# Performance work log

Hardware: AMD Instinct MI355X
Metric: run time of the kernel (lower is better)

## Reference

```python
import jax, jax.numpy as jnp
import numpy as np

B, N, M, C, H, D = 1, 4096, 4096, 768, 12, 64  # batch, tgt len, src len, in_dim, heads, head_dim
SCALE = D ** -0.5


def setup_inputs() -> dict:
    key = jax.random.key(0)
    ks = jax.random.split(key, 6)
    s = 0.02
    return {
        "x": jax.random.normal(ks[0], (B, N, C), jnp.float32),
        "src": jax.random.normal(ks[1], (B, M, C), jnp.float32),
        "W_qv": jax.random.normal(ks[2], (2 * H * D, C), jnp.float32) * s,
        "W_k": jax.random.normal(ks[3], (H * D, C), jnp.float32) * s,
        "W_proj": jax.random.normal(ks[4], (C, H * D), jnp.float32) * s,
        "b_proj": jnp.zeros((C,), jnp.float32),
    }


def reference(x, src, W_qv, W_k, W_proj, b_proj):
    Bb, Nn, _ = x.shape
    Mm = src.shape[1]
    # q, v come from src; k comes from x (info flows src -> target)
    qv = (src @ W_qv.T).reshape(Bb, Mm, 2, H, D)
    q = qv[:, :, 0].transpose(0, 2, 1, 3)  # (B, H, M, D)
    v = qv[:, :, 1].transpose(0, 2, 1, 3)  # (B, H, M, D)
    k = (x @ W_k.T).reshape(Bb, Nn, H, D) * SCALE  # (B, N, H, D), pre-scaled
    # attn[b,h,n,m] = q[b,h,m,:] . k[b,n,h,:]  (torch: (q @ k).transpose(-2,-1))
    attn = jnp.einsum('bhmd,bnhd->bhnm', q, k)
    attn = jax.nn.softmax(attn, axis=-1)  # softmax over src tokens m
    y = jnp.einsum('bhnm,bhmd->bnhd', attn, v).reshape(Bb, Nn, H * D)
    return y @ W_proj.T + b_proj
```

## Files before the change

### kernel.cpp

```cpp
#include <hip/hip_runtime.h>

using f32x4 = __attribute__((ext_vector_type(4))) float;
using f32x16 = __attribute__((ext_vector_type(16))) float;
using s16x8 = __attribute__((ext_vector_type(8))) short;
using u16x4 = __attribute__((ext_vector_type(4))) unsigned short;
using u32x4 = __attribute__((ext_vector_type(4))) unsigned int;

#define AS1 __attribute__((address_space(1)))
#define AS3 __attribute__((address_space(3)))

__device__ __forceinline__ void gload16(const void* g, void* l) {
  __builtin_amdgcn_global_load_lds((const AS1 unsigned int*)g,
                                   (AS3 unsigned int*)l, 16, 0, 0);
}

__device__ __forceinline__ unsigned short f2bf(float f) {
  unsigned int u = __builtin_bit_cast(unsigned int, f);
  u += 0x7fffu + ((u >> 16) & 1u);
  return (unsigned short)(u >> 16);
}

__device__ __forceinline__ float b2f(unsigned short u) {
  unsigned int x = ((unsigned int)u) << 16;
  return __builtin_bit_cast(float, x);
}

__device__ __forceinline__ unsigned int cvtpk(float lo, float hi) {
  unsigned int w;
  asm("v_cvt_pk_bf16_f32 %0, %1, %2" : "=v"(w) : "v"(lo), "v"(hi));
  return w;
}

__device__ __forceinline__ void plswap(unsigned int& a, unsigned int& b) {
  asm("v_permlane32_swap_b32 %0, %1" : "+v"(a), "+v"(b));
}

__global__ __launch_bounds__(256) void cvt_bf16_multi(
    const float* __restrict__ i0, const float* __restrict__ i1,
    const float* __restrict__ i2, const float* __restrict__ i3,
    const float* __restrict__ i4, unsigned short* __restrict__ o0,
    unsigned short* __restrict__ o1, unsigned short* __restrict__ o2,
    unsigned short* __restrict__ o3, unsigned short* __restrict__ o4) {
  int b = blockIdx.x;
  const float* in;
  unsigned short* out;
  int base, n4;
  if (b < 3072) { in = i0; out = o0; base = b; n4 = 786432; }
  else if (b < 6144) { in = i1; out = o1; base = b - 3072; n4 = 786432; }
  else if (b < 7296) { in = i2; out = o2; base = b - 6144; n4 = 294912; }
  else if (b < 7872) { in = i3; out = o3; base = b - 7296; n4 = 147456; }
  else { in = i4; out = o4; base = b - 7872; n4 = 147456; }
  int i = base * 256 + threadIdx.x;
  if (i >= n4) return;
  f32x4 v = ((const f32x4*)in)[i];
  u16x4 r;
#pragma unroll
  for (int j = 0; j < 4; ++j) r[j] = f2bf(v[j]);
  ((u16x4*)out)[i] = r;
}

__global__ __launch_bounds__(256) void gemm_proj(
    const unsigned short* __restrict__ srcb, const unsigned short* __restrict__ wqvb,
    const unsigned short* __restrict__ xb, const unsigned short* __restrict__ wkb,
    unsigned short* __restrict__ qbuf, unsigned short* __restrict__ vtbuf,
    unsigned short* __restrict__ kbuf) {
  __shared__ __align__(16) unsigned short As[128 * 64];
  __shared__ __align__(16) unsigned short Bs[128 * 64];
  const bool isqv = blockIdx.y < 12;
  const unsigned short* A = isqv ? srcb : xb;
  const unsigned short* B = isqv ? wqvb : wkb;
  const int n0 = (isqv ? blockIdx.y : (blockIdx.y - 12)) * 128;
  const int m0 = blockIdx.x * 128;
  const int t = threadIdx.x;
  const int lane = t & 63;
  const int wid = t >> 6;
  const int wr = wid >> 1, wc = wid & 1;
  const int fr = lane & 15, fq = lane >> 4;

  f32x4 acc[4][4];
#pragma unroll
  for (int i = 0; i < 4; ++i)
#pragma unroll
    for (int j = 0; j < 4; ++j) acc[i][j] = (f32x4){0.f, 0.f, 0.f, 0.f};

  const char* Ab = (const char*)A;
  const char* Bb = (const char*)B;

  for (int k0 = 0; k0 < 768; k0 += 64) {
#pragma unroll
    for (int p = 0; p < 4; ++p) {
      int idx = p * 256 + t;
      int row = idx >> 3;
      int scb = ((idx & 7) << 4) ^ ((row & 7) << 4);
      char* dstA = (char*)As + (p * 256 + (wid << 6)) * 16;
      char* dstB = (char*)Bs + (p * 256 + (wid << 6)) * 16;
      gload16(Ab + (size_t)(m0 + row) * 1536 + (size_t)k0 * 2 + scb, dstA);
      gload16(Bb + (size_t)(n0 + row) * 1536 + (size_t)k0 * 2 + scb, dstB);
    }
    __syncthreads();

    s16x8 af[4][2], bfr[4][2];
#pragma unroll
    for (int mi = 0; mi < 4; ++mi)
#pragma unroll
      for (int kk = 0; kk < 2; ++kk) {
        int row = wr * 64 + mi * 16 + fr;
        int cb = (kk * 64 + (fq << 4)) ^ ((row & 7) << 4);
        af[mi][kk] = *(const s16x8*)((const char*)As + row * 128 + cb);
      }
#pragma unroll
    for (int ni = 0; ni < 4; ++ni)
#pragma unroll
      for (int kk = 0; kk < 2; ++kk) {
        int row = wc * 64 + ni * 16 + fr;
        int cb = (kk * 64 + (fq << 4)) ^ ((row & 7) << 4);
        bfr[ni][kk] = *(const s16x8*)((const char*)Bs + row * 128 + cb);
      }
    __builtin_amdgcn_s_setprio(1);
#pragma unroll
    for (int kk = 0; kk < 2; ++kk)
#pragma unroll
      for (int mi = 0; mi < 4; ++mi)
#pragma unroll
        for (int ni = 0; ni < 4; ++ni)
          acc[mi][ni] = __builtin_amdgcn_mfma_f32_16x16x32_bf16(
              af[mi][kk], bfr[ni][kk], acc[mi][ni], 0, 0, 0);
    __builtin_amdgcn_s_setprio(0);
    __syncthreads();
  }

#pragma unroll
  for (int mi = 0; mi < 4; ++mi) {
#pragma unroll
    for (int ni = 0; ni < 4; ++ni) {
      int row0 = m0 + wr * 64 + mi * 16 + (fq << 2);
      int col = n0 + wc * 64 + ni * 16 + fr;
      if (isqv) {
        if (n0 < 768) {
#pragma unroll
          for (int j = 0; j < 4; ++j)
            qbuf[(size_t)(row0 + j) * 768 + col] = f2bf(acc[mi][ni][j]);
        } else {
          u16x4 pk;
#pragma unroll
          for (int j = 0; j < 4; ++j) pk[j] = f2bf(acc[mi][ni][j]);
          *(u16x4*)(vtbuf + (size_t)(col - 768) * 4096 + row0) = pk;
        }
      } else {
#pragma unroll
        for (int j = 0; j < 4; ++j)
          kbuf[(size_t)(row0 + j) * 768 + col] = f2bf(acc[mi][ni][j] * 0.18033688f);
      }
    }
  }
}

__global__ __launch_bounds__(256) void gemm_out(
    const unsigned short* __restrict__ A, const unsigned short* __restrict__ B,
    float* __restrict__ outp, const float* __restrict__ bias) {
  __shared__ __align__(16) unsigned short As[64 * 64];
  __shared__ __align__(16) unsigned short Bs[64 * 64];
  const int t = threadIdx.x;
  const int lane = t & 63;
  const int wid = t >> 6;
  const int wr = wid >> 1, wc = wid & 1;
  const int m0 = blockIdx.x * 64, n0 = blockIdx.y * 64;
  const int fr = lane & 15, fq = lane >> 4;

  f32x4 acc[2][2];
#pragma unroll
  for (int i = 0; i < 2; ++i)
#pragma unroll
    for (int j = 0; j < 2; ++j) acc[i][j] = (f32x4){0.f, 0.f, 0.f, 0.f};

  for (int k0 = 0; k0 < 768; k0 += 64) {
#pragma unroll
    for (int p = 0; p < 2; ++p) {
      int idx = p * 256 + t;
      int row = idx >> 3;
      int scb = ((idx & 7) << 4) ^ ((row & 7) << 4);
      char* dstA = (char*)As + (p * 256 + (wid << 6)) * 16;
      char* dstB = (char*)Bs + (p * 256 + (wid << 6)) * 16;
      gload16((const char*)A + (size_t)(m0 + row) * 1536 + (size_t)k0 * 2 + scb, dstA);
      gload16((const char*)B + (size_t)(n0 + row) * 1536 + (size_t)k0 * 2 + scb, dstB);
    }
    __syncthreads();

    s16x8 af[2][2], bfr[2][2];
#pragma unroll
    for (int mi = 0; mi < 2; ++mi)
#pragma unroll
      for (int kk = 0; kk < 2; ++kk) {
        int row = wr * 32 + mi * 16 + fr;
        int cb = (kk * 64 + (fq << 4)) ^ ((row & 7) << 4);
        af[mi][kk] = *(const s16x8*)((const char*)As + row * 128 + cb);
      }
#pragma unroll
    for (int ni = 0; ni < 2; ++ni)
#pragma unroll
      for (int kk = 0; kk < 2; ++kk) {
        int row = wc * 32 + ni * 16 + fr;
        int cb = (kk * 64 + (fq << 4)) ^ ((row & 7) << 4);
        bfr[ni][kk] = *(const s16x8*)((const char*)Bs + row * 128 + cb);
      }
    __builtin_amdgcn_s_setprio(1);
#pragma unroll
    for (int kk = 0; kk < 2; ++kk)
#pragma unroll
      for (int mi = 0; mi < 2; ++mi)
#pragma unroll
        for (int ni = 0; ni < 2; ++ni)
          acc[mi][ni] = __builtin_amdgcn_mfma_f32_16x16x32_bf16(
              af[mi][kk], bfr[ni][kk], acc[mi][ni], 0, 0, 0);
    __builtin_amdgcn_s_setprio(0);
    __syncthreads();
  }

#pragma unroll
  for (int mi = 0; mi < 2; ++mi) {
#pragma unroll
    for (int ni = 0; ni < 2; ++ni) {
      int row0 = m0 + wr * 32 + mi * 16 + (fq << 2);
      int col = n0 + wc * 32 + ni * 16 + fr;
      float bv = bias[col];
#pragma unroll
      for (int j = 0; j < 4; ++j)
        outp[(size_t)(row0 + j) * 768 + col] = acc[mi][ni][j] + bv;
    }
  }
}

__global__ __launch_bounds__(256, 3) void attn_kernel(
    const unsigned short* __restrict__ Qk, const unsigned short* __restrict__ Kq,
    const unsigned short* __restrict__ Vt, unsigned short* __restrict__ Po0,
    unsigned short* __restrict__ PoR, float* __restrict__ Pl) {
  __shared__ __align__(16) unsigned short Ks[3][64 * 64];
  __shared__ __align__(16) unsigned short Vs[3][64 * 64];
  const int t = threadIdx.x, lane = t & 63, wid = t >> 6;
  const int half = lane >> 5, l31 = lane & 31;

  int bid = blockIdx.x;
  int f = (bid & 7) * 192 + (bid >> 3);
  const int h = f >> 7;
  const int rem = f & 127;
  const int n0 = (rem >> 2) * 128;
  const int sp = rem & 3;
  const int mbase = sp * 1024;

  s16x8 qf[4];
  {
    const size_t qrow = n0 + wid * 32 + l31;
#pragma unroll
    for (int kc = 0; kc < 4; ++kc)
      qf[kc] = *(const s16x8*)(Qk + qrow * 768 + h * 64 + kc * 16 + half * 8);
  }

  f32x16 o[2];
#pragma unroll
  for (int dt = 0; dt < 2; ++dt)
#pragma unroll
    for (int r = 0; r < 16; ++r) o[dt][r] = 0.f;
  f32x16 lacc;
#pragma unroll
  for (int r = 0; r < 16; ++r) lacc[r] = 0.f;
  f32x16 z16;
#pragma unroll
  for (int r = 0; r < 16; ++r) z16[r] = 0.f;
  s16x8 ones;
#pragma unroll
  for (int i = 0; i < 8; ++i) ones[i] = (short)0x3F80;

  const int rswz = (l31 & 7) << 4;
  const int rbase = l31 * 128;
  int coff[4];
#pragma unroll
  for (int kc = 0; kc < 4; ++kc)
    coff[kc] = (kc * 32 + half * 16) ^ rswz;

  const int srow = t >> 3;
  const int sscb = ((t & 7) << 4) ^ ((srow & 7) << 4);
  const char* kp0 = (const char*)Kq + (size_t)(mbase + srow) * 1536 + h * 128 + sscb;
  const char* kp1 = kp0 + 49152;
  const char* vp0 = (const char*)Vt + (size_t)(h * 64 + srow) * 8192 +
                    (size_t)mbase * 2 + sscb;
  const char* vp1 = vp0 + 262144;
  const int ldst = wid << 10;

#pragma unroll
  for (int pb = 0; pb < 2; ++pb) {
    char* kd = (char*)Ks + pb * 8192 + ldst;
    char* vd = (char*)Vs + pb * 8192 + ldst;
    gload16(kp0, kd);
    gload16(kp1, kd + 4096);
    gload16(vp0, vd);
    gload16(vp1, vd + 4096);
    kp0 += 98304; kp1 += 98304; vp0 += 128; vp1 += 128;
  }

  int cur = 0;
  for (int it = 0; it < 16; ++it) {
    if (it < 15) {
      asm volatile("s_waitcnt vmcnt(4)" ::: "memory");
    } else {
      asm volatile("s_waitcnt vmcnt(0)" ::: "memory");
    }
    __builtin_amdgcn_s_barrier();
    __builtin_amdgcn_sched_barrier(0);

    if (it < 14) {
      int stg = cur + 2;
      if (stg >= 3) stg -= 3;
      char* kd = (char*)Ks + stg * 8192 + ldst;
      char* vd = (char*)Vs + stg * 8192 + ldst;
      gload16(kp0, kd);
      gload16(kp1, kd + 4096);
      gload16(vp0, vd);
      gload16(vp1, vd + 4096);
      kp0 += 98304; kp1 += 98304; vp0 += 128; vp1 += 128;
    }

    const char* Ksb = (const char*)Ks + cur * 8192;
    const char* Vsb = (const char*)Vs + cur * 8192;

    s16x8 pfrag[4];
#pragma unroll
    for (int mt = 0; mt < 2; ++mt) {
      f32x16 s;
      __builtin_amdgcn_s_setprio(1);
      {
        s16x8 kf = *(const s16x8*)(Ksb + mt * 4096 + rbase + coff[0]);
        s = __builtin_amdgcn_mfma_f32_32x32x16_bf16(kf, qf[0], z16, 0, 0, 0);
      }
#pragma unroll
      for (int kc = 1; kc < 4; ++kc) {
        s16x8 kf = *(const s16x8*)(Ksb + mt * 4096 + rbase + coff[kc]);
        s = __builtin_amdgcn_mfma_f32_32x32x16_bf16(kf, qf[kc], s, 0, 0, 0);
      }
      __builtin_amdgcn_s_setprio(0);

#pragma unroll
      for (int r = 0; r < 16; ++r) s[r] = __builtin_exp2f(s[r]);

      unsigned int w[8];
#pragma unroll
      for (int i = 0; i < 8; ++i) w[i] = cvtpk(s[2 * i], s[2 * i + 1]);
      plswap(w[0], w[2]);
      plswap(w[1], w[3]);
      plswap(w[4], w[6]);
      plswap(w[5], w[7]);
      u32x4 f0, f1;
      f0[0] = w[0]; f0[1] = w[1]; f0[2] = w[2]; f0[3] = w[3];
      f1[0] = w[4]; f1[1] = w[5]; f1[2] = w[6]; f1[3] = w[7];
      pfrag[2 * mt] = __builtin_bit_cast(s16x8, f0);
      pfrag[2 * mt + 1] = __builtin_bit_cast(s16x8, f1);

      __builtin_amdgcn_s_setprio(1);
      lacc = __builtin_amdgcn_mfma_f32_32x32x16_bf16(ones, pfrag[2 * mt], lacc, 0, 0, 0);
      lacc = __builtin_amdgcn_mfma_f32_32x32x16_bf16(ones, pfrag[2 * mt + 1], lacc, 0, 0, 0);
      __builtin_amdgcn_s_setprio(0);
    }

    __builtin_amdgcn_s_setprio(1);
#pragma unroll
    for (int dt = 0; dt < 2; ++dt)
#pragma unroll
      for (int kc = 0; kc < 4; ++kc) {
        s16x8 vf = *(const s16x8*)(Vsb + dt * 4096 + rbase + coff[kc]);
        o[dt] = __builtin_amdgcn_mfma_f32_32x32x16_bf16(vf, pfrag[kc], o[dt], 0, 0, 0);
      }
    __builtin_amdgcn_s_setprio(0);

    cur = (cur == 2) ? 0 : cur + 1;
  }

  float lsum = lacc[0];
  unsigned short* Po = (sp == 0) ? Po0 : (PoR + (size_t)(sp - 1) * 3145728);
  const size_t n = n0 + wid * 32 + l31;
  if (!half) Pl[sp * 49152 + n * 12 + h] = lsum;
#pragma unroll
  for (int dt = 0; dt < 2; ++dt)
#pragma unroll
    for (int g = 0; g < 4; ++g) {
      u16x4 pk;
#pragma unroll
      for (int e = 0; e < 4; ++e) pk[e] = f2bf(o[dt][4 * g + e]);
      int d = dt * 32 + 8 * g + 4 * half;
      *(u16x4*)(Po + n * 768 + h * 64 + d) = pk;
    }
}

__global__ __launch_bounds__(256) void attn_combine(
    const unsigned short* __restrict__ Po0, const unsigned short* __restrict__ PoR,
    const float* __restrict__ Pl, unsigned short* __restrict__ Y) {
  int idx = blockIdx.x * 256 + threadIdx.x;
  int row = idx / 192;
  int c4 = idx - row * 192;
  int col = c4 * 4;
  int h = col >> 6;
  float l = Pl[(size_t)row * 12 + h] + Pl[49152 + (size_t)row * 12 + h] +
            Pl[2 * 49152 + (size_t)row * 12 + h] +
            Pl[3 * 49152 + (size_t)row * 12 + h];
  float inv = 1.0f / l;
  size_t off = (size_t)row * 768 + col;
  u16x4 a = *(const u16x4*)(Po0 + off);
  u16x4 b = *(const u16x4*)(PoR + off);
  u16x4 c = *(const u16x4*)(PoR + 3145728 + off);
  u16x4 d = *(const u16x4*)(PoR + 2 * 3145728 + off);
  u16x4 r;
#pragma unroll
  for (int e = 0; e < 4; ++e) {
    float s = b2f(a[e]) + b2f(b[e]) + b2f(c[e]) + b2f(d[e]);
    r[e] = f2bf(s * inv);
  }
  *(u16x4*)(Y + (size_t)row * 768 + col) = r;
}

extern "C" void kernel_launch(void* const* d_in, const int* in_sizes, int n_in,
                              void* d_out, int out_size, void* d_ws,
                              size_t ws_size, hipStream_t stream) {
  const float* x = (const float*)d_in[0];
  const float* src = (const float*)d_in[1];
  const float* Wqv = (const float*)d_in[2];
  const float* Wk = (const float*)d_in[3];
  const float* Wp = (const float*)d_in[4];
  const float* bp = (const float*)d_in[5];
  float* out = (float*)d_out;

  char* ws = (char*)d_ws;
  unsigned short* srcb = (unsigned short*)(ws + 0);
  unsigned short* xb   = (unsigned short*)(ws + 6291456);
  unsigned short* wqvb = (unsigned short*)(ws + 12582912);
  unsigned short* wkb  = (unsigned short*)(ws + 14942208);
  unsigned short* wpb  = (unsigned short*)(ws + 16121856);
  unsigned short* qbuf = (unsigned short*)(ws + 17301504);
  unsigned short* vtbuf= (unsigned short*)(ws + 23592960);
  unsigned short* kbuf = (unsigned short*)(ws + 29884416);
  unsigned short* ybuf = (unsigned short*)(ws + 36175872);
  unsigned short* part0 = (unsigned short*)(ws + 0);
  float* lsums = (float*)(ws + 12582912);
  unsigned short* partR = (unsigned short*)(ws + 42467328);

  cvt_bf16_multi<<<8448, 256, 0, stream>>>(src, x, Wqv, Wk, Wp, srcb, xb, wqvb,
                                           wkb, wpb);

  gemm_proj<<<dim3(32, 18), 256, 0, stream>>>(srcb, wqvb, xb, wkb, qbuf, vtbuf,
                                              kbuf);
  attn_kernel<<<1536, 256, 0, stream>>>(kbuf, qbuf, vtbuf, part0, partR, lsums);
  attn_combine<<<3072, 256, 0, stream>>>(part0, partR, lsums, ybuf);
  gemm_out<<<dim3(64, 12), 256, 0, stream>>>(ybuf, wpb, out, bp);
}
```

Baseline: 143.4 us.

## Shrink projection GEMM tiles to 64x64 and double-buffer attention K/V

The projection GEMM moves from 128x128 to 64x64 output tiles, launching four times as many blocks (64x36 grid). This trades less reuse per block for more parallelism and lower LDS and register use. The attention kernel drops from a three-stage to a two-stage K/V LDS ring. Each tile is now waited on right after its prefetch is issued, with an extra barrier at the end of every iteration, so LDS use falls at the cost of less load/compute overlap and more synchronisation.

Result: faster. 138.5 us (median of 2 runs) (-3.4%).

```diff
diff --git a/kernel.cpp b/kernel.cpp
--- a/kernel.cpp
+++ b/kernel.cpp
@@ -64,55 +64,52 @@
     const unsigned short* __restrict__ xb, const unsigned short* __restrict__ wkb,
     unsigned short* __restrict__ qbuf, unsigned short* __restrict__ vtbuf,
     unsigned short* __restrict__ kbuf) {
-  __shared__ __align__(16) unsigned short As[128 * 64];
-  __shared__ __align__(16) unsigned short Bs[128 * 64];
-  const bool isqv = blockIdx.y < 12;
+  __shared__ __align__(16) unsigned short As[64 * 64];
+  __shared__ __align__(16) unsigned short Bs[64 * 64];
+  const bool isqv = blockIdx.y < 24;
   const unsigned short* A = isqv ? srcb : xb;
   const unsigned short* B = isqv ? wqvb : wkb;
-  const int n0 = (isqv ? blockIdx.y : (blockIdx.y - 12)) * 128;
-  const int m0 = blockIdx.x * 128;
+  const int n0 = (isqv ? blockIdx.y : (blockIdx.y - 24)) * 64;
+  const int m0 = blockIdx.x * 64;
   const int t = threadIdx.x;
   const int lane = t & 63;
   const int wid = t >> 6;
   const int wr = wid >> 1, wc = wid & 1;
   const int fr = lane & 15, fq = lane >> 4;
 
-  f32x4 acc[4][4];
-#pragma unroll
-  for (int i = 0; i < 4; ++i)
-#pragma unroll
-    for (int j = 0; j < 4; ++j) acc[i][j] = (f32x4){0.f, 0.f, 0.f, 0.f};
-
-  const char* Ab = (const char*)A;
-  const char* Bb = (const char*)B;
+  f32x4 acc[2][2];
+#pragma unroll
+  for (int i = 0; i < 2; ++i)
+#pragma unroll
+    for (int j = 0; j < 2; ++j) acc[i][j] = (f32x4){0.f, 0.f, 0.f, 0.f};
 
   for (int k0 = 0; k0 < 768; k0 += 64) {
 #pragma unroll
-    for (int p = 0; p < 4; ++p) {
+    for (int p = 0; p < 2; ++p) {
       int idx = p * 256 + t;
       int row = idx >> 3;
       int scb = ((idx & 7) << 4) ^ ((row & 7) << 4);
       char* dstA = (char*)As + (p * 256 + (wid << 6)) * 16;
       char* dstB = (char*)Bs + (p * 256 + (wid << 6)) * 16;
-      gload16(Ab + (size_t)(m0 + row) * 1536 + (size_t)k0 * 2 + scb, dstA);
-      gload16(Bb + (size_t)(n0 + row) * 1536 + (size_t)k0 * 2 + scb, dstB);
+      gload16((const char*)A + (size_t)(m0 + row) * 1536 + (size_t)k0 * 2 + scb, dstA);
+      gload16((const char*)B + (size_t)(n0 + row) * 1536 + (size_t)k0 * 2 + scb, dstB);
     }
     __syncthreads();
 
-    s16x8 af[4][2], bfr[4][2];
-#pragma unroll
-    for (int mi = 0; mi < 4; ++mi)
+    s16x8 af[2][2], bfr[2][2];
+#pragma unroll
+    for (int mi = 0; mi < 2; ++mi)
 #pragma unroll
       for (int kk = 0; kk < 2; ++kk) {
-        int row = wr * 64 + mi * 16 + fr;
+        int row = wr * 32 + mi * 16 + fr;
         int cb = (kk * 64 + (fq << 4)) ^ ((row & 7) << 4);
         af[mi][kk] = *(const s16x8*)((const char*)As + row * 128 + cb);
       }
 #pragma unroll
-    for (int ni = 0; ni < 4; ++ni)
+    for (int ni = 0; ni < 2; ++ni)
 #pragma unroll
       for (int kk = 0; kk < 2; ++kk) {
-        int row = wc * 64 + ni * 16 + fr;
+        int row = wc * 32 + ni * 16 + fr;
         int cb = (kk * 64 + (fq << 4)) ^ ((row & 7) << 4);
         bfr[ni][kk] = *(const s16x8*)((const char*)Bs + row * 128 + cb);
       }
@@ -120,9 +117,9 @@
 #pragma unroll
     for (int kk = 0; kk < 2; ++kk)
 #pragma unroll
-      for (int mi = 0; mi < 4; ++mi)
-#pragma unroll
-        for (int ni = 0; ni < 4; ++ni)
+      for (int mi = 0; mi < 2; ++mi)
+#pragma unroll
+        for (int ni = 0; ni < 2; ++ni)
           acc[mi][ni] = __builtin_amdgcn_mfma_f32_16x16x32_bf16(
               af[mi][kk], bfr[ni][kk], acc[mi][ni], 0, 0, 0);
     __builtin_amdgcn_s_setprio(0);
@@ -130,13 +127,13 @@
   }
 
 #pragma unroll
-  for (int mi = 0; mi < 4; ++mi) {
-#pragma unroll
-    for (int ni = 0; ni < 4; ++ni) {
-      int row0 = m0 + wr * 64 + mi * 16 + (fq << 2);
-      int col = n0 + wc * 64 + ni * 16 + fr;
+  for (int mi = 0; mi < 2; ++mi) {
+#pragma unroll
+    for (int ni = 0; ni < 2; ++ni) {
+      int row0 = m0 + wr * 32 + mi * 16 + (fq << 2);
+      int col = n0 + wc * 32 + ni * 16 + fr;
       if (isqv) {
-        if (n0 < 768) {
+        if (col < 768) {
 #pragma unroll
           for (int j = 0; j < 4; ++j)
             qbuf[(size_t)(row0 + j) * 768 + col] = f2bf(acc[mi][ni][j]);
@@ -234,8 +231,8 @@
     const unsigned short* __restrict__ Qk, const unsigned short* __restrict__ Kq,
     const unsigned short* __restrict__ Vt, unsigned short* __restrict__ Po0,
     unsigned short* __restrict__ PoR, float* __restrict__ Pl) {
-  __shared__ __align__(16) unsigned short Ks[3][64 * 64];
-  __shared__ __align__(16) unsigned short Vs[3][64 * 64];
+  __shared__ __align__(16) unsigned short Ks[2][64 * 64];
+  __shared__ __align__(16) unsigned short Vs[2][64 * 64];
   const int t = threadIdx.x, lane = t & 63, wid = t >> 6;
   const int half = lane >> 5, l31 = lane & 31;
 
@@ -286,41 +283,38 @@
   const char* vp1 = vp0 + 262144;
   const int ldst = wid << 10;
 
-#pragma unroll
-  for (int pb = 0; pb < 2; ++pb) {
-    char* kd = (char*)Ks + pb * 8192 + ldst;
-    char* vd = (char*)Vs + pb * 8192 + ldst;
+  {
+    char* kd = (char*)Ks[0] + ldst;
+    char* vd = (char*)Vs[0] + ldst;
     gload16(kp0, kd);
     gload16(kp1, kd + 4096);
     gload16(vp0, vd);
     gload16(vp1, vd + 4096);
     kp0 += 98304; kp1 += 98304; vp0 += 128; vp1 += 128;
   }
-
-  int cur = 0;
+  asm volatile("s_waitcnt vmcnt(0)" ::: "memory");
+  __builtin_amdgcn_s_barrier();
+  __builtin_amdgcn_sched_barrier(0);
+
   for (int it = 0; it < 16; ++it) {
+    const int buf = it & 1;
     if (it < 15) {
-      asm volatile("s_waitcnt vmcnt(4)" ::: "memory");
-    } else {
-      asm volatile("s_waitcnt vmcnt(0)" ::: "memory");
-    }
-    __builtin_amdgcn_s_barrier();
-    __builtin_amdgcn_sched_barrier(0);
-
-    if (it < 14) {
-      int stg = cur + 2;
-      if (stg >= 3) stg -= 3;
-      char* kd = (char*)Ks + stg * 8192 + ldst;
-      char* vd = (char*)Vs + stg * 8192 + ldst;
+      char* kd = (char*)Ks[buf ^ 1] + ldst;
+      char* vd = (char*)Vs[buf ^ 1] + ldst;
       gload16(kp0, kd);
       gload16(kp1, kd + 4096);
       gload16(vp0, vd);
       gload16(vp1, vd + 4096);
       kp0 += 98304; kp1 += 98304; vp0 += 128; vp1 += 128;
-    }
-
-    const char* Ksb = (const char*)Ks + cur * 8192;
-    const char* Vsb = (const char*)Vs + cur * 8192;
+      asm volatile("s_waitcnt vmcnt(4)" ::: "memory");
+    } else {
+      asm volatile("s_waitcnt vmcnt(0)" ::: "memory");
+    }
+    __builtin_amdgcn_s_barrier();
+    __builtin_amdgcn_sched_barrier(0);
+
+    const char* Ksb = (const char*)Ks[buf];
+    const char* Vsb = (const char*)Vs[buf];
 
     s16x8 pfrag[4];
 #pragma unroll
@@ -369,8 +363,8 @@
         o[dt] = __builtin_amdgcn_mfma_f32_32x32x16_bf16(vf, pfrag[kc], o[dt], 0, 0, 0);
       }
     __builtin_amdgcn_s_setprio(0);
-
-    cur = (cur == 2) ? 0 : cur + 1;
+    __builtin_amdgcn_s_barrier();
+    __builtin_amdgcn_sched_barrier(0);
   }
 
   float lsum = lacc[0];
@@ -443,7 +437,7 @@
   cvt_bf16_multi<<<8448, 256, 0, stream>>>(src, x, Wqv, Wk, Wp, srcb, xb, wqvb,
                                            wkb, wpb);
 
-  gemm_proj<<<dim3(32, 18), 256, 0, stream>>>(srcb, wqvb, xb, wkb, qbuf, vtbuf,
+  gemm_proj<<<dim3(64, 36), 256, 0, stream>>>(srcb, wqvb, xb, wkb, qbuf, vtbuf,
                                               kbuf);
   attn_kernel<<<1536, 256, 0, stream>>>(kbuf, qbuf, vtbuf, part0, partR, lsums);
   attn_combine<<<3072, 256, 0, stream>>>(part0, partR, lsums, ybuf);
```
